# Kernel optimization log

Measured on AMD Instinct MI355X. Metric: run time of the kernel, lower is better.

The kernel has to match this reference:

```python
import jax, jax.numpy as jnp
import numpy as np

TEXT_DIM, GIN = 5000, 128
B, N, E = 4096, 200000, 6400000
AE_HID, AE_EMB, G_HID, G_EMB = 8, 4, 8, 4


def _gcn(x, W, b, src, dst):
    N_ = x.shape[0]
    h = x @ W
    loop = jnp.arange(N_)
    s = jnp.concatenate([src, loop])
    d = jnp.concatenate([dst, loop])
    deg = jax.ops.segment_sum(jnp.ones(s.shape[0], h.dtype), d, num_segments=N_)
    dinv = jnp.where(deg > 0, jax.lax.rsqrt(jnp.maximum(deg, 1e-12)), 0.0)
    norm = dinv[s] * dinv[d]
    out = jax.ops.segment_sum(h[s] * norm[:, None], d, num_segments=N_)
    return out + b


def setup_inputs() -> dict:
    key = jax.random.key(0)
    ks = jax.random.split(key, 20)
    def lin(k, fan_in, fan_out):
        lim = 1.0 / np.sqrt(fan_in)
        kw, kb = jax.random.split(k)
        W = jax.random.uniform(kw, (fan_in, fan_out), jnp.float32, -lim, lim)
        b = jax.random.uniform(kb, (fan_out,), jnp.float32, -lim, lim)
        return W, b
    W_e1, b_e1 = lin(ks[0], TEXT_DIM, AE_HID)
    W_e2, b_e2 = lin(ks[1], AE_HID, AE_EMB)
    W_d1, b_d1 = lin(ks[2], AE_EMB, AE_HID)
    W_d2, b_d2 = lin(ks[3], AE_HID, TEXT_DIM)
    W_g1, b_g1 = lin(ks[4], GIN, G_HID)
    W_g2, b_g2 = lin(ks[5], G_HID, G_EMB)
    W_c, b_c = lin(ks[6], AE_EMB + G_EMB, 1)
    text_x = jax.random.normal(ks[7], (B, TEXT_DIM), jnp.float32)
    node_x = jax.random.normal(ks[8], (N, GIN), jnp.float32)
    edge_index = jax.random.randint(ks[9], (2, E), 0, N, jnp.int64 if jax.config.jax_enable_x64 else jnp.int32)
    batch = jnp.sort(jax.random.randint(ks[10], (N,), 0, B, edge_index.dtype))
    return {"text_x": text_x, "node_x": node_x, "edge_index": edge_index, "batch": batch,
            "W_e1": W_e1, "b_e1": b_e1, "W_e2": W_e2, "b_e2": b_e2,
            "W_d1": W_d1, "b_d1": b_d1, "W_d2": W_d2, "b_d2": b_d2,
            "W_g1": W_g1, "b_g1": b_g1, "W_g2": W_g2, "b_g2": b_g2,
            "W_c": W_c, "b_c": b_c}


def reference(text_x, node_x, edge_index, batch,
              W_e1, b_e1, W_e2, b_e2, W_d1, b_d1, W_d2, b_d2,
              W_g1, b_g1, W_g2, b_g2, W_c, b_c):
    # Autoencoder (eval mode: dropout = identity)
    z_text = jax.nn.relu(jax.nn.relu(text_x @ W_e1 + b_e1) @ W_e2 + b_e2)
    x_hat = jax.nn.sigmoid(jax.nn.relu(z_text @ W_d1 + b_d1) @ W_d2 + b_d2)
    # GNN encoder
    src, dst = edge_index[0], edge_index[1]
    h = jax.nn.relu(_gcn(node_x, W_g1, b_g1, src, dst))
    h = _gcn(h, W_g2, b_g2, src, dst)
    # global mean pool over graphs
    nb = text_x.shape[0]
    sums = jax.ops.segment_sum(h, batch, num_segments=nb)
    cnt = jax.ops.segment_sum(jnp.ones(h.shape[0], h.dtype), batch, num_segments=nb)
    z_graph = sums / jnp.maximum(cnt, 1.0)[:, None]
    z = jnp.concatenate([z_text, z_graph], axis=1)
    logits = z @ W_c + b_c
    return (x_hat, logits, z)
```

## Files before the change

kernel.cpp:

```cpp
#include <hip/hip_runtime.h>

#define BB 4096
#define TD 5000
#define NN 200000
#define EE 6400000
#define NBK 782

__global__ void k_init(const int* __restrict__ e, unsigned int* __restrict__ deg,
                       int* __restrict__ flag) {
    int i = blockIdx.x * 256 + threadIdx.x;
    if (i < NN) deg[i] = 1u;
    if (blockIdx.x == 0) {
        __shared__ int r[256];
        int tid = threadIdx.x;
        int acc = 0;
        for (int k = tid; k < 4096; k += 256) acc |= e[2 * k + 1];
        r[tid] = acc;
        __syncthreads();
        for (int s = 128; s > 0; s >>= 1) {
            if (tid < s) r[tid] |= r[tid + s];
            __syncthreads();
        }
        if (tid == 0) *flag = (r[0] == 0) ? 1 : 0;
    }
}

__global__ __launch_bounds__(256) void k_rank_enc(
    const int* __restrict__ edge, const int* __restrict__ flag,
    unsigned int* __restrict__ deg, unsigned int* __restrict__ rnk,
    const float* __restrict__ text,
    const float* __restrict__ We1, const float* __restrict__ be1,
    const float* __restrict__ We2, const float* __restrict__ be2,
    float* __restrict__ z_text)
{
    __shared__ float red[8][256];
    __shared__ float t1[8];
    int bid = blockIdx.x, tid = threadIdx.x;
    int enc_id = -1, rank_id = -1;
    if (bid < 6250) {
        if (bid & 1) enc_id = bid >> 1;
        else rank_id = bid >> 1;
    } else {
        enc_id = 3125 + (bid - 6250);
    }

    if (rank_id >= 0) {
        int f = *flag;
        int base = rank_id * 2048 + tid;
        int d[8];
#pragma unroll
        for (int k = 0; k < 8; k++) {
            int e = base + k * 256;
            d[k] = f ? edge[2 * (EE + e)] : edge[EE + e];
        }
        unsigned int rr[8];
#pragma unroll
        for (int k = 0; k < 8; k++) rr[k] = atomicAdd(&deg[d[k]], 1u);
#pragma unroll
        for (int k = 0; k < 8; k++) rnk[base + k * 256] = rr[k];
        return;
    }

    int row = enc_id;
    const float4* xrow = (const float4*)(text + (size_t)row * TD);
    float acc[8];
#pragma unroll
    for (int j = 0; j < 8; j++) acc[j] = 0.f;
    for (int v = tid; v < 1250; v += 256) {
        float4 xv = xrow[v];
        const float4* w = (const float4*)(We1 + (size_t)v * 32);
        float xc[4] = {xv.x, xv.y, xv.z, xv.w};
#pragma unroll
        for (int c = 0; c < 4; c++) {
            float4 wa = w[c * 2], wb = w[c * 2 + 1];
            acc[0] += xc[c] * wa.x; acc[1] += xc[c] * wa.y;
            acc[2] += xc[c] * wa.z; acc[3] += xc[c] * wa.w;
            acc[4] += xc[c] * wb.x; acc[5] += xc[c] * wb.y;
            acc[6] += xc[c] * wb.z; acc[7] += xc[c] * wb.w;
        }
    }
#pragma unroll
    for (int j = 0; j < 8; j++) red[j][tid] = acc[j];
    __syncthreads();
    for (int s = 128; s > 0; s >>= 1) {
        if (tid < s) {
#pragma unroll
            for (int j = 0; j < 8; j++) red[j][tid] += red[j][tid + s];
        }
        __syncthreads();
    }
    if (tid < 8) t1[tid] = fmaxf(red[tid][0] + be1[tid], 0.f);
    __syncthreads();
    if (tid < 4) {
        float z = be2[tid];
#pragma unroll
        for (int k = 0; k < 8; k++) z += t1[k] * We2[k * 4 + tid];
        z_text[row * 4 + tid] = fmaxf(z, 0.f);
    }
}

__global__ void kA_all(const unsigned int* __restrict__ deg, float* __restrict__ dinv,
                       unsigned int* __restrict__ bsum, const int* __restrict__ batch,
                       const int* __restrict__ flag, unsigned int* __restrict__ bnd) {
    __shared__ unsigned int s[256];
    int tid = threadIdx.x;
    int i = blockIdx.x * 256 + tid;
    unsigned int c = 0u;
    if (i < NN) {
        unsigned int u = deg[i];
        dinv[i] = rsqrtf((float)u);
        c = u - 1u;
        int fg = *flag;
        int b = fg ? batch[2 * i] : batch[i];
        int bp = (i == 0) ? -1 : (fg ? batch[2 * (i - 1)] : batch[i - 1]);
        for (int bb = bp + 1; bb <= b; bb++) bnd[bb] = (unsigned int)i;
        if (i == NN - 1)
            for (int bb = b + 1; bb <= BB; bb++) bnd[bb] = (unsigned int)NN;
    }
    s[tid] = c;
    __syncthreads();
    for (int st = 128; st > 0; st >>= 1) {
        if (tid < st) s[tid] += s[tid + st];
        __syncthreads();
    }
    if (tid == 0) bsum[blockIdx.x] = s[0];
}

__global__ void kB_scanblocks(const unsigned int* __restrict__ bsum, unsigned int* __restrict__ bpre,
                              unsigned int* __restrict__ indptr) {
    __shared__ unsigned int s[1024];
    int t = threadIdx.x;
    s[t] = (t < NBK) ? bsum[t] : 0u;
    __syncthreads();
    for (int off = 1; off < 1024; off <<= 1) {
        unsigned int v = (t >= off) ? s[t - off] : 0u;
        __syncthreads();
        s[t] += v;
        __syncthreads();
    }
    if (t < NBK) bpre[t] = (t == 0) ? 0u : s[t - 1];
    if (t == 0) indptr[NN] = EE;
}

__global__ void kC_indptr(const unsigned int* __restrict__ deg, const unsigned int* __restrict__ bpre,
                          unsigned int* __restrict__ indptr) {
    __shared__ unsigned int s[256];
    int tid = threadIdx.x;
    int i = blockIdx.x * 256 + tid;
    unsigned int c = (i < NN) ? (deg[i] - 1u) : 0u;
    s[tid] = c;
    __syncthreads();
    for (int off = 1; off < 256; off <<= 1) {
        unsigned int v = (tid >= off) ? s[tid - off] : 0u;
        __syncthreads();
        s[tid] += v;
        __syncthreads();
    }
    if (i < NN) indptr[i] = bpre[blockIdx.x] + s[tid] - c;
}

__global__ void k_place(const int* __restrict__ edge, const int* __restrict__ flag,
                        const unsigned int* __restrict__ indptr, const unsigned int* __restrict__ rnk,
                        int* __restrict__ csr) {
    int f = *flag;
    int base = blockIdx.x * 1024 + threadIdx.x;
    int s[4], d[4];
#pragma unroll
    for (int k = 0; k < 4; k++) {
        int e = base + k * 256;
        s[k] = f ? edge[2 * e] : edge[e];
        d[k] = f ? edge[2 * (EE + e)] : edge[EE + e];
    }
    unsigned int rr[4];
#pragma unroll
    for (int k = 0; k < 4; k++) rr[k] = rnk[base + k * 256];
    unsigned int ip[4];
#pragma unroll
    for (int k = 0; k < 4; k++) ip[k] = indptr[d[k]];
#pragma unroll
    for (int k = 0; k < 4; k++) csr[ip[k] + rr[k] - 1u] = s[k];
}

__global__ __launch_bounds__(256) void k_gcn1_mm(
    const float* __restrict__ nodex, const float* __restrict__ Wg1,
    const float* __restrict__ dinv, float* __restrict__ h0g)
{
    __shared__ float W[128 * 8];
    int tid = threadIdx.x;
    for (int i = tid; i < 1024; i += 256) W[i] = Wg1[i];
    __syncthreads();
    int row = blockIdx.x * 256 + tid;
    if (row >= NN) return;
    const float4* xr = (const float4*)(nodex + (size_t)row * 128);
    float acc[8];
#pragma unroll
    for (int j = 0; j < 8; j++) acc[j] = 0.f;
#pragma unroll 8
    for (int c = 0; c < 32; c++) {
        float4 v = xr[c];
        const float* wr = &W[c * 32];
#pragma unroll
        for (int j = 0; j < 8; j++)
            acc[j] += v.x * wr[j] + v.y * wr[8 + j] + v.z * wr[16 + j] + v.w * wr[24 + j];
    }
    float di = dinv[row];
    float* o = h0g + (size_t)row * 8;
#pragma unroll
    for (int j = 0; j < 8; j++) o[j] = di * acc[j];
}

__global__ __launch_bounds__(256) void k_gather1(
    const unsigned int* __restrict__ indptr, const int* __restrict__ csr_src,
    const float* __restrict__ h0g, const float* __restrict__ dinv,
    const float* __restrict__ bg1, const float* __restrict__ Wg2,
    float* __restrict__ h2g)
{
    __shared__ float W[32];
    __shared__ float b1[8];
    __shared__ float h1s[4][8];
    int tid = threadIdx.x;
    if (tid < 32) W[tid] = Wg2[tid];
    if (tid < 8) b1[tid] = bg1[tid];
    __syncthreads();
    int wid = tid >> 6, lane = tid & 63;
    int i = blockIdx.x * 4 + wid;
    if (i < NN) {
        int beg = indptr[i], end = indptr[i + 1];
        int f = lane & 7;
        float a = 0.f;
        for (int k = beg + (lane >> 3); k < end; k += 8)
            a += h0g[(size_t)csr_src[k] * 8 + f];
        a += __shfl_xor(a, 8, 64);
        a += __shfl_xor(a, 16, 64);
        a += __shfl_xor(a, 32, 64);
        if (lane < 8) {
            float di = dinv[i];
            h1s[wid][f] = fmaxf(di * (a + h0g[(size_t)i * 8 + f]) + b1[f], 0.f);
        }
    }
    __syncthreads();
    if (i < NN && lane < 4) {
        float di = dinv[i];
        float s = 0.f;
#pragma unroll
        for (int k = 0; k < 8; k++) s += h1s[wid][k] * W[k * 4 + lane];
        h2g[(size_t)i * 4 + lane] = di * s;
    }
}

__global__ __launch_bounds__(256) void k_gather2(
    const unsigned int* __restrict__ indptr, const int* __restrict__ csr_src,
    const float* __restrict__ h2g, const float* __restrict__ dinv,
    const float* __restrict__ bg2, float* __restrict__ h2f)
{
    __shared__ float b2[4];
    int tid = threadIdx.x;
    if (tid < 4) b2[tid] = bg2[tid];
    __syncthreads();
    int wid = tid >> 6, lane = tid & 63;
    int i = blockIdx.x * 4 + wid;
    if (i >= NN) return;
    int beg = indptr[i], end = indptr[i + 1];
    int f = lane & 3;
    float a = 0.f;
    for (int k = beg + (lane >> 2); k < end; k += 16)
        a += h2g[(size_t)csr_src[k] * 4 + f];
    a += __shfl_xor(a, 4, 64);
    a += __shfl_xor(a, 8, 64);
    a += __shfl_xor(a, 16, 64);
    a += __shfl_xor(a, 32, 64);
    if (lane < 4) {
        float di = dinv[i];
        h2f[(size_t)i * 4 + f] = di * (a + h2g[(size_t)i * 4 + f]) + b2[f];
    }
}

__global__ __launch_bounds__(256) void k_final(
    const float* __restrict__ h2f, const unsigned int* __restrict__ bnd,
    const float* __restrict__ z_text, const float* __restrict__ Wc,
    const float* __restrict__ bc, float* __restrict__ out_logits,
    float* __restrict__ out_z)
{
    __shared__ float red[256][4];
    int g = blockIdx.x, tid = threadIdx.x;
    int lo = bnd[g], hi = bnd[g + 1];
    float a0 = 0.f, a1 = 0.f, a2 = 0.f, a3 = 0.f;
    for (int i = lo + tid; i < hi; i += 256) {
        float4 v = *(const float4*)(h2f + (size_t)i * 4);
        a0 += v.x; a1 += v.y; a2 += v.z; a3 += v.w;
    }
    red[tid][0] = a0; red[tid][1] = a1; red[tid][2] = a2; red[tid][3] = a3;
    __syncthreads();
    for (int s = 128; s > 0; s >>= 1) {
        if (tid < s) {
            red[tid][0] += red[tid + s][0]; red[tid][1] += red[tid + s][1];
            red[tid][2] += red[tid + s][2]; red[tid][3] += red[tid + s][3];
        }
        __syncthreads();
    }
    if (tid == 0) {
        float c = (float)(hi - lo);
        c = fmaxf(c, 1.f);
        float z8[8];
#pragma unroll
        for (int j = 0; j < 4; j++) z8[j] = z_text[g * 4 + j];
#pragma unroll
        for (int j = 0; j < 4; j++) z8[4 + j] = red[0][j] / c;
        float l = bc[0];
#pragma unroll
        for (int k = 0; k < 8; k++) l += z8[k] * Wc[k];
        out_logits[g] = l;
#pragma unroll
        for (int k = 0; k < 8; k++) out_z[g * 8 + k] = z8[k];
    }
}

__global__ __launch_bounds__(256) void k_ae_decode(
    const float* __restrict__ out_z,
    const float* __restrict__ Wd1, const float* __restrict__ bd1,
    const float* __restrict__ Wd2, const float* __restrict__ bd2,
    float* __restrict__ xhat)
{
    int row = blockIdx.x, tid = threadIdx.x;
    float zz[4];
#pragma unroll
    for (int j = 0; j < 4; j++) zz[j] = out_z[row * 8 + j];
    float t[8];
#pragma unroll
    for (int k = 0; k < 8; k++) {
        float s = bd1[k];
#pragma unroll
        for (int j = 0; j < 4; j++) s += zz[j] * Wd1[j * 8 + k];
        t[k] = fmaxf(s, 0.f);
    }
    float4* orow = (float4*)(xhat + (size_t)row * TD);
    for (int c4 = tid; c4 < 1250; c4 += 256) {
        float4 s = *(const float4*)(bd2 + c4 * 4);
#pragma unroll
        for (int k = 0; k < 8; k++) {
            float4 w = *(const float4*)(Wd2 + (size_t)k * TD + c4 * 4);
            s.x += t[k] * w.x; s.y += t[k] * w.y;
            s.z += t[k] * w.z; s.w += t[k] * w.w;
        }
        s.x = 1.f / (1.f + expf(-s.x));
        s.y = 1.f / (1.f + expf(-s.y));
        s.z = 1.f / (1.f + expf(-s.z));
        s.w = 1.f / (1.f + expf(-s.w));
        orow[c4] = s;
    }
}

extern "C" void kernel_launch(void* const* d_in, const int* in_sizes, int n_in,
                              void* d_out, int out_size, void* d_ws, size_t ws_size,
                              hipStream_t stream) {
    const float* text  = (const float*)d_in[0];
    const float* nodex = (const float*)d_in[1];
    const int* edge    = (const int*)d_in[2];
    const int* batch   = (const int*)d_in[3];
    const float* We1 = (const float*)d_in[4];
    const float* be1 = (const float*)d_in[5];
    const float* We2 = (const float*)d_in[6];
    const float* be2 = (const float*)d_in[7];
    const float* Wd1 = (const float*)d_in[8];
    const float* bd1 = (const float*)d_in[9];
    const float* Wd2 = (const float*)d_in[10];
    const float* bd2 = (const float*)d_in[11];
    const float* Wg1 = (const float*)d_in[12];
    const float* bg1 = (const float*)d_in[13];
    const float* Wg2 = (const float*)d_in[14];
    const float* bg2 = (const float*)d_in[15];
    const float* Wc  = (const float*)d_in[16];
    const float* bc  = (const float*)d_in[17];

    char* sc = (char*)d_out;
    float*        h0g    = (float*)(sc + 0);
    float*        h2g    = (float*)(sc + 6400000);
    float*        h2f    = (float*)(sc + 9600000);
    float*        dinv   = (float*)(sc + 12800000);
    unsigned int* deg    = (unsigned int*)(sc + 13600000);
    unsigned int* indptr = (unsigned int*)(sc + 14400000);
    unsigned int* rnk    = (unsigned int*)(sc + 15200004);
    int*          csr    = (int*)(sc + 40800004);
    unsigned int* bsum   = (unsigned int*)(sc + 66400004);
    unsigned int* bpre   = (unsigned int*)(sc + 66403132);
    float*        z_text = (float*)(sc + 66406260);
    unsigned int* bnd    = (unsigned int*)(sc + 66471796);
    int*          flag   = (int*)(sc + 66488184);

    float* out_xhat   = (float*)d_out;
    float* out_logits = out_xhat + (size_t)BB * TD;
    float* out_z      = out_logits + BB;

    k_init<<<NBK, 256, 0, stream>>>(edge, deg, flag);
    k_rank_enc<<<7221, 256, 0, stream>>>(edge, flag, deg, rnk,
                                         text, We1, be1, We2, be2, z_text);
    kA_all<<<NBK, 256, 0, stream>>>(deg, dinv, bsum, batch, flag, bnd);
    kB_scanblocks<<<1, 1024, 0, stream>>>(bsum, bpre, indptr);
    kC_indptr<<<NBK, 256, 0, stream>>>(deg, bpre, indptr);
    k_place<<<6250, 256, 0, stream>>>(edge, flag, indptr, rnk, csr);

    k_gcn1_mm<<<NBK, 256, 0, stream>>>(nodex, Wg1, dinv, h0g);
    k_gather1<<<(NN + 3) / 4, 256, 0, stream>>>(indptr, csr, h0g, dinv, bg1, Wg2, h2g);
    k_gather2<<<(NN + 3) / 4, 256, 0, stream>>>(indptr, csr, h2g, dinv, bg2, h2f);

    k_final<<<BB, 256, 0, stream>>>(h2f, bnd, z_text, Wc, bc, out_logits, out_z);
    k_ae_decode<<<BB, 256, 0, stream>>>(out_z, Wd1, bd1, Wd2, bd2, out_xhat);
}
```

Measured before the change: 723.1 us.

## Fuse independent stages into multi-role kernels and move scratch to workspace

Merges the node feature matmul into the rank/encoder kernel, and interleaves CSR placement, dinv scaling and the autoencoder decode in a second fused kernel. The dinv scaling is split out of the matmul because dinv is not yet known when the matmul runs. Scratch buffers move to the workspace when it is large enough, which lets the decode run early from z_text without waiting for the final pooling. This removes launches and overlaps memory-bound and atomic-bound work across stages. In exchange it adds an extra pass over h0g and more shared-memory pressure in the fat kernels.

```diff
diff --git a/kernel.cpp b/kernel.cpp
--- a/kernel.cpp
+++ b/kernel.cpp
@@ -5,6 +5,7 @@
 #define NN 200000
 #define EE 6400000
 #define NBK 782
+#define WS_NEED 66488188ull
 
 __global__ void k_init(const int* __restrict__ e, unsigned int* __restrict__ deg,
                        int* __restrict__ flag) {
@@ -25,43 +26,30 @@
     }
 }
 
-__global__ __launch_bounds__(256) void k_rank_enc(
-    const int* __restrict__ edge, const int* __restrict__ flag,
-    unsigned int* __restrict__ deg, unsigned int* __restrict__ rnk,
-    const float* __restrict__ text,
-    const float* __restrict__ We1, const float* __restrict__ be1,
-    const float* __restrict__ We2, const float* __restrict__ be2,
-    float* __restrict__ z_text)
-{
+__device__ void role_rank(int rid, int tid, const int* __restrict__ edge,
+                          const int* __restrict__ flag, unsigned int* __restrict__ deg,
+                          unsigned int* __restrict__ rnk) {
+    int f = *flag;
+    int base = rid * 2048 + tid;
+    int d[8];
+#pragma unroll
+    for (int k = 0; k < 8; k++) {
+        int e = base + k * 256;
+        d[k] = f ? edge[2 * (EE + e)] : edge[EE + e];
+    }
+    unsigned int rr[8];
+#pragma unroll
+    for (int k = 0; k < 8; k++) rr[k] = atomicAdd(&deg[d[k]], 1u);
+#pragma unroll
+    for (int k = 0; k < 8; k++) rnk[base + k * 256] = rr[k];
+}
+
+__device__ void role_enc(int row, int tid, const float* __restrict__ text,
+                         const float* __restrict__ We1, const float* __restrict__ be1,
+                         const float* __restrict__ We2, const float* __restrict__ be2,
+                         float* __restrict__ z_text) {
     __shared__ float red[8][256];
     __shared__ float t1[8];
-    int bid = blockIdx.x, tid = threadIdx.x;
-    int enc_id = -1, rank_id = -1;
-    if (bid < 6250) {
-        if (bid & 1) enc_id = bid >> 1;
-        else rank_id = bid >> 1;
-    } else {
-        enc_id = 3125 + (bid - 6250);
-    }
-
-    if (rank_id >= 0) {
-        int f = *flag;
-        int base = rank_id * 2048 + tid;
-        int d[8];
-#pragma unroll
-        for (int k = 0; k < 8; k++) {
-            int e = base + k * 256;
-            d[k] = f ? edge[2 * (EE + e)] : edge[EE + e];
-        }
-        unsigned int rr[8];
-#pragma unroll
-        for (int k = 0; k < 8; k++) rr[k] = atomicAdd(&deg[d[k]], 1u);
-#pragma unroll
-        for (int k = 0; k < 8; k++) rnk[base + k * 256] = rr[k];
-        return;
-    }
-
-    int row = enc_id;
     const float4* xrow = (const float4*)(text + (size_t)row * TD);
     float acc[8];
 #pragma unroll
@@ -97,6 +85,151 @@
         for (int k = 0; k < 8; k++) z += t1[k] * We2[k * 4 + tid];
         z_text[row * 4 + tid] = fmaxf(z, 0.f);
     }
+}
+
+__device__ void role_mm(int mid, int tid, const float* __restrict__ nodex,
+                        const float* __restrict__ Wg1, float* __restrict__ h0g) {
+    __shared__ float W[1024];
+    for (int i = tid; i < 1024; i += 256) W[i] = Wg1[i];
+    __syncthreads();
+    int row = mid * 256 + tid;
+    if (row >= NN) return;
+    const float4* xr = (const float4*)(nodex + (size_t)row * 128);
+    float acc[8];
+#pragma unroll
+    for (int j = 0; j < 8; j++) acc[j] = 0.f;
+#pragma unroll 8
+    for (int c = 0; c < 32; c++) {
+        float4 v = xr[c];
+        const float* wr = &W[c * 32];
+#pragma unroll
+        for (int j = 0; j < 8; j++)
+            acc[j] += v.x * wr[j] + v.y * wr[8 + j] + v.z * wr[16 + j] + v.w * wr[24 + j];
+    }
+    float* o = h0g + (size_t)row * 8;
+#pragma unroll
+    for (int j = 0; j < 8; j++) o[j] = acc[j];
+}
+
+__device__ void role_place(int pid, int tid, const int* __restrict__ edge,
+                           const int* __restrict__ flag, const unsigned int* __restrict__ indptr,
+                           const unsigned int* __restrict__ rnk, int* __restrict__ csr) {
+    int f = *flag;
+    int base = pid * 1024 + tid;
+    int s[4], d[4];
+#pragma unroll
+    for (int k = 0; k < 4; k++) {
+        int e = base + k * 256;
+        s[k] = f ? edge[2 * e] : edge[e];
+        d[k] = f ? edge[2 * (EE + e)] : edge[EE + e];
+    }
+    unsigned int rr[4];
+#pragma unroll
+    for (int k = 0; k < 4; k++) rr[k] = rnk[base + k * 256];
+    unsigned int ip[4];
+#pragma unroll
+    for (int k = 0; k < 4; k++) ip[k] = indptr[d[k]];
+#pragma unroll
+    for (int k = 0; k < 4; k++) csr[ip[k] + rr[k] - 1u] = s[k];
+}
+
+__device__ void role_scale(int sid, int tid, float* __restrict__ h0g,
+                           const float* __restrict__ dinv) {
+    int i = sid * 256 + tid;
+    if (i >= NN) return;
+    float di = dinv[i];
+    float4* p = (float4*)(h0g + (size_t)i * 8);
+    float4 a = p[0], b = p[1];
+    a.x *= di; a.y *= di; a.z *= di; a.w *= di;
+    b.x *= di; b.y *= di; b.z *= di; b.w *= di;
+    p[0] = a; p[1] = b;
+}
+
+__device__ void role_decode(int row, int tid, const float* __restrict__ zsrc, int zstride,
+                            const float* __restrict__ Wd1, const float* __restrict__ bd1,
+                            const float* __restrict__ Wd2, const float* __restrict__ bd2,
+                            float* __restrict__ xhat) {
+    float zz[4];
+#pragma unroll
+    for (int j = 0; j < 4; j++) zz[j] = zsrc[row * zstride + j];
+    float t[8];
+#pragma unroll
+    for (int k = 0; k < 8; k++) {
+        float s = bd1[k];
+#pragma unroll
+        for (int j = 0; j < 4; j++) s += zz[j] * Wd1[j * 8 + k];
+        t[k] = fmaxf(s, 0.f);
+    }
+    float4* orow = (float4*)(xhat + (size_t)row * TD);
+    for (int c4 = tid; c4 < 1250; c4 += 256) {
+        float4 s = *(const float4*)(bd2 + c4 * 4);
+#pragma unroll
+        for (int k = 0; k < 8; k++) {
+            float4 w = *(const float4*)(Wd2 + (size_t)k * TD + c4 * 4);
+            s.x += t[k] * w.x; s.y += t[k] * w.y;
+            s.z += t[k] * w.z; s.w += t[k] * w.w;
+        }
+        s.x = 1.f / (1.f + expf(-s.x));
+        s.y = 1.f / (1.f + expf(-s.y));
+        s.z = 1.f / (1.f + expf(-s.z));
+        s.w = 1.f / (1.f + expf(-s.w));
+        orow[c4] = s;
+    }
+}
+
+__global__ __launch_bounds__(256) void k_fat1(
+    const int* __restrict__ edge, const int* __restrict__ flag,
+    unsigned int* __restrict__ deg, unsigned int* __restrict__ rnk,
+    const float* __restrict__ text,
+    const float* __restrict__ We1, const float* __restrict__ be1,
+    const float* __restrict__ We2, const float* __restrict__ be2,
+    float* __restrict__ z_text,
+    const float* __restrict__ nodex, const float* __restrict__ Wg1,
+    float* __restrict__ h0g)
+{
+    int bid = blockIdx.x, tid = threadIdx.x;
+    if (bid < 6250) {
+        if (bid & 1) role_enc(bid >> 1, tid, text, We1, be1, We2, be2, z_text);
+        else role_rank(bid >> 1, tid, edge, flag, deg, rnk);
+    } else if (bid < 7221) {
+        role_enc(3125 + (bid - 6250), tid, text, We1, be1, We2, be2, z_text);
+    } else {
+        role_mm(bid - 7221, tid, nodex, Wg1, h0g);
+    }
+}
+
+__global__ __launch_bounds__(256) void k_fat2(
+    const int* __restrict__ edge, const int* __restrict__ flag,
+    const unsigned int* __restrict__ indptr, const unsigned int* __restrict__ rnk,
+    int* __restrict__ csr, float* __restrict__ h0g, const float* __restrict__ dinv,
+    const float* __restrict__ zsrc, int zstride,
+    const float* __restrict__ Wd1, const float* __restrict__ bd1,
+    const float* __restrict__ Wd2, const float* __restrict__ bd2,
+    float* __restrict__ xhat, int ndec)
+{
+    int bid = blockIdx.x, tid = threadIdx.x;
+    if (ndec > 0) {
+        if (bid < 8192) {
+            if (bid & 1) role_decode(bid >> 1, tid, zsrc, zstride, Wd1, bd1, Wd2, bd2, xhat);
+            else role_place(bid >> 1, tid, edge, flag, indptr, rnk, csr);
+        } else if (bid < 10346) {
+            role_place(4096 + (bid - 8192), tid, edge, flag, indptr, rnk, csr);
+        } else {
+            role_scale(bid - 10346, tid, h0g, dinv);
+        }
+    } else {
+        if (bid < 6250) role_place(bid, tid, edge, flag, indptr, rnk, csr);
+        else role_scale(bid - 6250, tid, h0g, dinv);
+    }
+}
+
+__global__ __launch_bounds__(256) void k_dec(
+    const float* __restrict__ zsrc, int zstride,
+    const float* __restrict__ Wd1, const float* __restrict__ bd1,
+    const float* __restrict__ Wd2, const float* __restrict__ bd2,
+    float* __restrict__ xhat)
+{
+    role_decode(blockIdx.x, threadIdx.x, zsrc, zstride, Wd1, bd1, Wd2, bd2, xhat);
 }
 
 __global__ void kA_all(const unsigned int* __restrict__ deg, float* __restrict__ dinv,
@@ -159,56 +292,6 @@
     if (i < NN) indptr[i] = bpre[blockIdx.x] + s[tid] - c;
 }
 
-__global__ void k_place(const int* __restrict__ edge, const int* __restrict__ flag,
-                        const unsigned int* __restrict__ indptr, const unsigned int* __restrict__ rnk,
-                        int* __restrict__ csr) {
-    int f = *flag;
-    int base = blockIdx.x * 1024 + threadIdx.x;
-    int s[4], d[4];
-#pragma unroll
-    for (int k = 0; k < 4; k++) {
-        int e = base + k * 256;
-        s[k] = f ? edge[2 * e] : edge[e];
-        d[k] = f ? edge[2 * (EE + e)] : edge[EE + e];
-    }
-    unsigned int rr[4];
-#pragma unroll
-    for (int k = 0; k < 4; k++) rr[k] = rnk[base + k * 256];
-    unsigned int ip[4];
-#pragma unroll
-    for (int k = 0; k < 4; k++) ip[k] = indptr[d[k]];
-#pragma unroll
-    for (int k = 0; k < 4; k++) csr[ip[k] + rr[k] - 1u] = s[k];
-}
-
-__global__ __launch_bounds__(256) void k_gcn1_mm(
-    const float* __restrict__ nodex, const float* __restrict__ Wg1,
-    const float* __restrict__ dinv, float* __restrict__ h0g)
-{
-    __shared__ float W[128 * 8];
-    int tid = threadIdx.x;
-    for (int i = tid; i < 1024; i += 256) W[i] = Wg1[i];
-    __syncthreads();
-    int row = blockIdx.x * 256 + tid;
-    if (row >= NN) return;
-    const float4* xr = (const float4*)(nodex + (size_t)row * 128);
-    float acc[8];
-#pragma unroll
-    for (int j = 0; j < 8; j++) acc[j] = 0.f;
-#pragma unroll 8
-    for (int c = 0; c < 32; c++) {
-        float4 v = xr[c];
-        const float* wr = &W[c * 32];
-#pragma unroll
-        for (int j = 0; j < 8; j++)
-            acc[j] += v.x * wr[j] + v.y * wr[8 + j] + v.z * wr[16 + j] + v.w * wr[24 + j];
-    }
-    float di = dinv[row];
-    float* o = h0g + (size_t)row * 8;
-#pragma unroll
-    for (int j = 0; j < 8; j++) o[j] = di * acc[j];
-}
-
 __global__ __launch_bounds__(256) void k_gather1(
     const unsigned int* __restrict__ indptr, const int* __restrict__ csr_src,
     const float* __restrict__ h0g, const float* __restrict__ dinv,
@@ -312,41 +395,6 @@
         out_logits[g] = l;
 #pragma unroll
         for (int k = 0; k < 8; k++) out_z[g * 8 + k] = z8[k];
-    }
-}
-
-__global__ __launch_bounds__(256) void k_ae_decode(
-    const float* __restrict__ out_z,
-    const float* __restrict__ Wd1, const float* __restrict__ bd1,
-    const float* __restrict__ Wd2, const float* __restrict__ bd2,
-    float* __restrict__ xhat)
-{
-    int row = blockIdx.x, tid = threadIdx.x;
-    float zz[4];
-#pragma unroll
-    for (int j = 0; j < 4; j++) zz[j] = out_z[row * 8 + j];
-    float t[8];
-#pragma unroll
-    for (int k = 0; k < 8; k++) {
-        float s = bd1[k];
-#pragma unroll
-        for (int j = 0; j < 4; j++) s += zz[j] * Wd1[j * 8 + k];
-        t[k] = fmaxf(s, 0.f);
-    }
-    float4* orow = (float4*)(xhat + (size_t)row * TD);
-    for (int c4 = tid; c4 < 1250; c4 += 256) {
-        float4 s = *(const float4*)(bd2 + c4 * 4);
-#pragma unroll
-        for (int k = 0; k < 8; k++) {
-            float4 w = *(const float4*)(Wd2 + (size_t)k * TD + c4 * 4);
-            s.x += t[k] * w.x; s.y += t[k] * w.y;
-            s.z += t[k] * w.z; s.w += t[k] * w.w;
-        }
-        s.x = 1.f / (1.f + expf(-s.x));
-        s.y = 1.f / (1.f + expf(-s.y));
-        s.z = 1.f / (1.f + expf(-s.z));
-        s.w = 1.f / (1.f + expf(-s.w));
-        orow[c4] = s;
     }
 }
 
@@ -372,7 +420,9 @@
     const float* Wc  = (const float*)d_in[16];
     const float* bc  = (const float*)d_in[17];
 
-    char* sc = (char*)d_out;
+    const bool use_ws = (ws_size >= WS_NEED);
+    char* sc = use_ws ? (char*)d_ws : (char*)d_out;
+
     float*        h0g    = (float*)(sc + 0);
     float*        h2g    = (float*)(sc + 6400000);
     float*        h2f    = (float*)(sc + 9600000);
@@ -392,17 +442,27 @@
     float* out_z      = out_logits + BB;
 
     k_init<<<NBK, 256, 0, stream>>>(edge, deg, flag);
-    k_rank_enc<<<7221, 256, 0, stream>>>(edge, flag, deg, rnk,
-                                         text, We1, be1, We2, be2, z_text);
+    k_fat1<<<8003, 256, 0, stream>>>(edge, flag, deg, rnk,
+                                     text, We1, be1, We2, be2, z_text,
+                                     nodex, Wg1, h0g);
     kA_all<<<NBK, 256, 0, stream>>>(deg, dinv, bsum, batch, flag, bnd);
     kB_scanblocks<<<1, 1024, 0, stream>>>(bsum, bpre, indptr);
     kC_indptr<<<NBK, 256, 0, stream>>>(deg, bpre, indptr);
-    k_place<<<6250, 256, 0, stream>>>(edge, flag, indptr, rnk, csr);
-
-    k_gcn1_mm<<<NBK, 256, 0, stream>>>(nodex, Wg1, dinv, h0g);
+
+    if (use_ws) {
+        k_fat2<<<11128, 256, 0, stream>>>(edge, flag, indptr, rnk, csr, h0g, dinv,
+                                          z_text, 4, Wd1, bd1, Wd2, bd2, out_xhat, 4096);
+    } else {
+        k_fat2<<<7032, 256, 0, stream>>>(edge, flag, indptr, rnk, csr, h0g, dinv,
+                                         (const float*)nullptr, 0, Wd1, bd1, Wd2, bd2,
+                                         (float*)nullptr, 0);
+    }
+
     k_gather1<<<(NN + 3) / 4, 256, 0, stream>>>(indptr, csr, h0g, dinv, bg1, Wg2, h2g);
     k_gather2<<<(NN + 3) / 4, 256, 0, stream>>>(indptr, csr, h2g, dinv, bg2, h2f);
-
     k_final<<<BB, 256, 0, stream>>>(h2f, bnd, z_text, Wc, bc, out_logits, out_z);
-    k_ae_decode<<<BB, 256, 0, stream>>>(out_z, Wd1, bd1, Wd2, bd2, out_xhat);
-}
+
+    if (!use_ws) {
+        k_dec<<<BB, 256, 0, stream>>>(out_z, 8, Wd1, bd1, Wd2, bd2, out_xhat);
+    }
+}
```

New measurement: 739.6 us. 1.02x slower.
